# Optimization experiments

Hardware: AMD Instinct MI355X
Metric: run time of the kernel (lower is better)

Reference implementation:

```python
import jax, jax.numpy as jnp
import numpy as np

C = 96          # channels (= output_dim)
NUM_HEADS = 6
DILS = (1, 2, 3)
KS_ATT = 3      # dilate-attention kernel size
KS_COR = 5      # self-correlation kernel size
PAD_COR = 2
LN_EPS = 1e-5


def _unfold(x, k, dil, pad):
    # torch.nn.Unfold(kernel=k, dilation=dil, padding=pad, stride=1)
    # x: [B, C, H, W] -> [B, C, k*k, H, W] (channel-major, kernel row-major)
    B, c, H, W = x.shape
    xp = jnp.pad(x, ((0, 0), (0, 0), (pad, pad), (pad, pad)))
    patches = [xp[:, :, i * dil:i * dil + H, j * dil:j * dil + W]
               for i in range(k) for j in range(k)]
    return jnp.stack(patches, axis=2)


def _layernorm(x, g, b):
    m = jnp.mean(x, axis=-1, keepdims=True)
    v = jnp.mean((x - m) ** 2, axis=-1, keepdims=True)
    return (x - m) * jax.lax.rsqrt(v + LN_EPS) * g + b


def _dilate_attn(q, k, v, dil, head_dim, scale):
    # q,k,v: [B, cb, H, W] with cb = C // num_dilation
    B, cb, H, W = q.shape
    heads = cb // head_dim
    qf = q.reshape(B, heads, head_dim, H * W)                                  # bhdn
    kp = _unfold(k, KS_ATT, dil, dil).reshape(B, heads, head_dim, KS_ATT * KS_ATT, H * W)
    attn = jax.nn.softmax(jnp.einsum('bhdn,bhdkn->bhnk', qf, kp) * scale, axis=-1)
    vp = _unfold(v, KS_ATT, dil, dil).reshape(B, heads, head_dim, KS_ATT * KS_ATT, H * W)
    out = jnp.einsum('bhnk,bhdkn->bnhd', attn, vp)                             # [B,HW,heads,hd]
    return out.reshape(B, H, W, cb)


def _forward(x, g1, b1, Wqkv, bqkv, Wproj, bproj, g2, b2, W1, bm1, W2, bm2):
    B, Cc, H, W = x.shape
    nd = len(DILS)
    head_dim = Cc // NUM_HEADS
    scale = head_dim ** (-0.5)

    xh = jnp.transpose(x, (0, 2, 3, 1))                                        # [B,H,W,C]

    # --- MultiDilatelocalAttention block ---
    y = _layernorm(xh, g1, b1)
    qkv = jnp.einsum('bhwc,oc->bhwo', y, Wqkv) + bqkv                          # 1x1 conv == linear
    qkv = jnp.transpose(qkv, (0, 3, 1, 2)).reshape(B, 3, nd, Cc // nd, H, W)
    outs = []
    for i, d in enumerate(DILS):
        outs.append(_dilate_attn(qkv[:, 0, i], qkv[:, 1, i], qkv[:, 2, i], d, head_dim, scale))
    a = jnp.concatenate(outs, axis=-1)                                         # dilation-major channels
    a = a @ Wproj.T + bproj
    xh = xh + a

    # --- MLP block ---
    z = _layernorm(xh, g2, b2)
    z = jax.nn.gelu(z @ W1.T + bm1, approximate=False) @ W2.T + bm2
    xh = xh + z

    # --- self-correlation ---
    xc = jnp.transpose(xh, (0, 3, 1, 2))                                       # [B,C,H,W]
    xc = jax.nn.relu(xc)
    nrm = jnp.sqrt(jnp.sum(xc * xc, axis=1, keepdims=True))
    xc = xc / jnp.maximum(nrm, 1e-12)                                          # F.normalize dim=1
    pat = _unfold(xc, KS_COR, 1, PAD_COR)                                      # [B,C,25,H,W]
    out = pat.reshape(B, Cc, KS_COR, KS_COR, H, W) * xc[:, :, None, None]
    return jnp.transpose(out, (0, 1, 4, 5, 2, 3))                              # [B,C,H,W,5,5]


def setup_inputs() -> dict:
    key = jax.random.key(0)
    ks = jax.random.split(key, 8)
    B, H, W = 8, 64, 64
    s = 0.02
    return {
        'x': jax.random.normal(ks[0], (B, C, H, W), jnp.float32),
        'g1': jnp.ones((C,), jnp.float32),
        'b1': jnp.zeros((C,), jnp.float32),
        'Wqkv': jax.random.normal(ks[1], (3 * C, C), jnp.float32) * s,
        'bqkv': jnp.zeros((3 * C,), jnp.float32),
        'Wproj': jax.random.normal(ks[2], (C, C), jnp.float32) * s,
        'bproj': jnp.zeros((C,), jnp.float32),
        'g2': jnp.ones((C,), jnp.float32),
        'b2': jnp.zeros((C,), jnp.float32),
        'W1': jax.random.normal(ks[3], (4 * C, C), jnp.float32) * s,
        'bm1': jnp.zeros((4 * C,), jnp.float32),
        'W2': jax.random.normal(ks[4], (C, 4 * C), jnp.float32) * s,
        'bm2': jnp.zeros((C,), jnp.float32),
    }


def reference(x, g1, b1, Wqkv, bqkv, Wproj, bproj, g2, b2, W1, bm1, W2, bm2):
    return _forward(x, g1, b1, Wqkv, bqkv, Wproj, bproj, g2, b2, W1, bm1, W2, bm2)
```

## Files before the change

kernel.cpp:

```cpp
#include <hip/hip_runtime.h>
#include <math.h>

#define NN 4096
#define BN 32768
#define CSTR 66

using short8 = __attribute__((ext_vector_type(8))) short;
using f32x4  = __attribute__((ext_vector_type(4))) float;
typedef unsigned short ushort_t;

__device__ inline unsigned f2bfu(float f) {
    unsigned u = __builtin_bit_cast(unsigned, f);
    u += 0x7FFFu + ((u >> 16) & 1u);
    return u >> 16;
}
__device__ inline ushort_t f2bf(float f) { return (ushort_t)f2bfu(f); }
__device__ inline unsigned pack2(float a, float b) { return f2bfu(a) | (f2bfu(b) << 16); }
__device__ inline float bflo(unsigned u) { return __builtin_bit_cast(float, u << 16); }
__device__ inline float bfhi(unsigned u) { return __builtin_bit_cast(float, u & 0xFFFF0000u); }

__device__ inline float gelu_f(float v) {
    float xx = v * 0.70710678118654752f;
    float a  = fabsf(xx);
    float t  = 1.0f / (1.0f + 0.3275911f * a);
    float p  = t*(0.254829592f + t*(-0.284496736f + t*(1.421413741f + t*(-1.453152027f + t*1.061405429f))));
    float erfv = 1.0f - p * __expf(-xx*xx);
    erfv = copysignf(erfv, xx);
    return 0.5f * v * (1.0f + erfv);
}

__device__ inline void stage_w(const unsigned* __restrict__ wbf, int stage,
                               ushort_t* dst, int wv, int lane) {
    const unsigned* src = wbf + (long)stage * 5120 + lane * 4;
    #pragma unroll
    for (int i = 0; i < 5; ++i) {
        int chunk = wv + 4 * i;
        __builtin_amdgcn_global_load_lds(
            (const __attribute__((address_space(1))) unsigned*)(src + chunk * 256),
            (__attribute__((address_space(3))) unsigned*)(dst + chunk * 512),
            16, 0, 0);
    }
}

__device__ inline float dotk16(const unsigned* kv, const float* q) {
    const uint4 a = *(const uint4*)kv;
    const uint4 b = *(const uint4*)(kv + 4);
    float l;
    l  = q[0]*bflo(a.x)  + q[1]*bfhi(a.x);
    l += q[2]*bflo(a.y)  + q[3]*bfhi(a.y);
    l += q[4]*bflo(a.z)  + q[5]*bfhi(a.z);
    l += q[6]*bflo(a.w)  + q[7]*bfhi(a.w);
    l += q[8]*bflo(b.x)  + q[9]*bfhi(b.x);
    l += q[10]*bflo(b.y) + q[11]*bfhi(b.y);
    l += q[12]*bflo(b.z) + q[13]*bfhi(b.z);
    l += q[14]*bflo(b.w) + q[15]*bfhi(b.w);
    return l;
}
__device__ inline void accv16(const unsigned* kv, float wgt, float* o) {
    const uint4 a = *(const uint4*)kv;
    const uint4 b = *(const uint4*)(kv + 4);
    o[0]  += wgt*bflo(a.x);  o[1]  += wgt*bfhi(a.x);
    o[2]  += wgt*bflo(a.y);  o[3]  += wgt*bfhi(a.y);
    o[4]  += wgt*bflo(a.z);  o[5]  += wgt*bfhi(a.z);
    o[6]  += wgt*bflo(a.w);  o[7]  += wgt*bfhi(a.w);
    o[8]  += wgt*bflo(b.x);  o[9]  += wgt*bfhi(b.x);
    o[10] += wgt*bflo(b.y);  o[11] += wgt*bfhi(b.y);
    o[12] += wgt*bflo(b.z);  o[13] += wgt*bfhi(b.z);
    o[14] += wgt*bflo(b.w);  o[15] += wgt*bfhi(b.w);
}

#define MFMA_GEMM6(ACC, APTR, BPTR)                                              \
    _Pragma("unroll")                                                            \
    for (int kc = 0; kc < 3; ++kc) {                                             \
        short8 a_ = *(const short8*)&(APTR)[(wv*16 + ln)*104 + kc*32 + qd*8];    \
        _Pragma("unroll")                                                        \
        for (int t = 0; t < 6; ++t) {                                            \
            short8 b_ = *(const short8*)&(BPTR)[(t*16 + ln)*104 + kc*32 + qd*8]; \
            ACC[t] = __builtin_amdgcn_mfma_f32_16x16x32_bf16(a_, b_, ACC[t], 0, 0, 0); \
        }                                                                        \
    }

__global__ __launch_bounds__(256) void k0_pack(
    const float* __restrict__ Wqkv, const float* __restrict__ Wproj,
    const float* __restrict__ W1, const float* __restrict__ W2,
    unsigned* __restrict__ wbf)
{
    int d = blockIdx.x * 256 + threadIdx.x;
    int s = d / 5120, r = d - s * 5120;
    int o = r / 52, qp = r - o * 52;
    unsigned val = 0u;
    if (o < 96 && qp < 48) {
        int q = qp * 2;
        float2 w2;
        if (s == 0)      w2 = *(const float2*)&Wqkv[(long)o * 96 + q];
        else if (s == 1) w2 = *(const float2*)&Wqkv[(long)(96 + o) * 96 + q];
        else if (s == 2) w2 = *(const float2*)&Wqkv[(long)(192 + o) * 96 + q];
        else if (s == 3) w2 = *(const float2*)&Wproj[(long)o * 96 + q];
        else if (((s - 4) & 1) == 0) { int kb = (s - 4) >> 1; w2 = *(const float2*)&W1[(long)(kb * 96 + o) * 96 + q]; }
        else                         { int kb = (s - 4) >> 1; w2 = *(const float2*)&W2[(long)o * 384 + kb * 96 + q]; }
        val = pack2(w2.x, w2.y);
    }
    wbf[d] = val;
}

__global__ __launch_bounds__(256, 2) void k1_ln_qkv(
    const float* __restrict__ x, const float* __restrict__ g1, const float* __restrict__ b1,
    const float* __restrict__ bqkv, const unsigned* __restrict__ wbf,
    unsigned* __restrict__ kvt32, unsigned* __restrict__ qimg)
{
    __shared__ __align__(16) float    Cs[96 * CSTR];
    __shared__ __align__(16) ushort_t As[64 * 104];
    __shared__ __align__(16) ushort_t Bs[2][10240];
    __shared__ float lnm[64], lnr[64];
    const int tid = threadIdx.x;
    const int bid = blockIdx.x;
    const int wg  = ((bid & 7) << 6) | (bid >> 3);
    const long bn0 = (long)wg << 6;
    const int b  = (int)(bn0 >> 12);
    const int n0 = (int)(bn0 & 4095);
    const int lane = tid & 63, wv = tid >> 6;
    const int ln = lane & 15, qd = lane >> 4;

    stage_w(wbf, 0, &Bs[0][0], wv, lane);
    stage_w(wbf, 1, &Bs[1][0], wv, lane);
    for (int i = 0; i < 6; ++i) {
        int idx = i * 256 + tid;
        int c = idx >> 4, p4 = idx & 15;
        float4 v = *(const float4*)&x[((long)(b * 96 + c) << 12) + n0 + p4 * 4];
        float* dst = &Cs[c * CSTR + p4 * 4];
        dst[0] = v.x; dst[1] = v.y; dst[2] = v.z; dst[3] = v.w;
    }
    __syncthreads();
    {
        int p = tid >> 2, part = tid & 3, c0 = part * 24;
        float s = 0.f, ss = 0.f;
        for (int c = c0; c < c0 + 24; ++c) { float v = Cs[c*CSTR + p]; s += v; ss += v*v; }
        s  += __shfl_xor(s, 1);  s  += __shfl_xor(s, 2);
        ss += __shfl_xor(ss, 1); ss += __shfl_xor(ss, 2);
        float m = s * (1.f/96.f);
        float rstd = rsqrtf(ss * (1.f/96.f) - m*m + 1e-5f);
        if (part == 0) { lnm[p] = m; lnr[p] = rstd; }
    }
    __syncthreads();
    for (int i = 0; i < 12; ++i) {
        int idx = i * 256 + tid;
        int p = idx / 48, cp = idx % 48;
        float m = lnm[p], rs = lnr[p];
        int c = 2 * cp;
        *(unsigned*)&As[p * 104 + 2*cp] =
            pack2((Cs[c*CSTR + p]     - m) * rs * g1[c]   + b1[c],
                  (Cs[(c+1)*CSTR + p] - m) * rs * g1[c+1] + b1[c+1]);
    }
    __syncthreads();
    f32x4 acc[6];
    #pragma unroll
    for (int t = 0; t < 6; ++t) acc[t] = (f32x4){0.f,0.f,0.f,0.f};
    MFMA_GEMM6(acc, As, Bs[0]);
    #pragma unroll
    for (int t = 0; t < 6; ++t)
        #pragma unroll
        for (int r = 0; r < 4; ++r)
            Cs[(t*16 + ln)*CSTR + (wv*16 + qd*4 + r)] = acc[t][r];
    __syncthreads();
    stage_w(wbf, 2, &Bs[0][0], wv, lane);
    for (int i = 0; i < 13; ++i) {
        int idx = i * 256 + tid;
        int p = idx / 52, cp = idx - p * 52;
        unsigned val = 0u;
        if (cp < 48) {
            int c = 2 * cp;
            val = pack2(Cs[c*CSTR + p] + bqkv[c], Cs[(c+1)*CSTR + p] + bqkv[c+1]);
        }
        qimg[(long)wg * 3328 + idx] = val;
    }
    #pragma unroll
    for (int t = 0; t < 6; ++t) acc[t] = (f32x4){0.f,0.f,0.f,0.f};
    MFMA_GEMM6(acc, As, Bs[1]);
    __syncthreads();
    #pragma unroll
    for (int t = 0; t < 6; ++t)
        #pragma unroll
        for (int r = 0; r < 4; ++r)
            Cs[(t*16 + ln)*CSTR + (wv*16 + qd*4 + r)] = acc[t][r];
    __syncthreads();
    for (int i = 0; i < 12; ++i) {
        int idx = i * 256 + tid;
        int p = idx / 48, cp = idx % 48;
        int c = 2 * cp;
        kvt32[(bn0 + p) * 96 + cp] =
            pack2(Cs[c*CSTR + p] + bqkv[96 + c], Cs[(c+1)*CSTR + p] + bqkv[96 + c + 1]);
    }
    #pragma unroll
    for (int t = 0; t < 6; ++t) acc[t] = (f32x4){0.f,0.f,0.f,0.f};
    MFMA_GEMM6(acc, As, Bs[0]);
    __syncthreads();
    #pragma unroll
    for (int t = 0; t < 6; ++t)
        #pragma unroll
        for (int r = 0; r < 4; ++r)
            Cs[(t*16 + ln)*CSTR + (wv*16 + qd*4 + r)] = acc[t][r];
    __syncthreads();
    for (int i = 0; i < 12; ++i) {
        int idx = i * 256 + tid;
        int p = idx / 48, cp = idx % 48;
        int c = 2 * cp;
        kvt32[(bn0 + p) * 96 + 48 + cp] =
            pack2(Cs[c*CSTR + p] + bqkv[192 + c], Cs[(c+1)*CSTR + p] + bqkv[192 + c + 1]);
    }
}

__global__ __launch_bounds__(256, 2) void k2345(
    const unsigned* __restrict__ kvt32, const unsigned* __restrict__ qimg,
    const float* __restrict__ x, const unsigned* __restrict__ wbf,
    const float* __restrict__ bproj,
    const float* __restrict__ g2, const float* __restrict__ b2,
    const float* __restrict__ bm1, const float* __restrict__ bm2,
    float* __restrict__ xcn)
{
    __shared__ __align__(16) float    Cs[96 * CSTR];
    __shared__ __align__(16) ushort_t As[64 * 104];
    __shared__ __align__(16) ushort_t Bs[2][10240];
    __shared__ float lnm[64], lnr[64];
    ushort_t* Hs = (ushort_t*)Cs;
    const int tid = threadIdx.x;
    const int bid = blockIdx.x;
    const int wg  = ((bid & 7) << 6) | (bid >> 3);
    const long bn0 = (long)wg << 6;
    const int b  = (int)(bn0 >> 12);
    const int n0 = (int)(bn0 & 4095);
    const int h0 = n0 >> 6;
    const int lane = tid & 63, wv = tid >> 6;
    const int ln = lane & 15, qd = lane >> 4;

    stage_w(wbf, 3, &Bs[0][0], wv, lane);
    stage_w(wbf, 4, &Bs[1][0], wv, lane);
    {
        const unsigned* src = qimg + (long)wg * 3328 + lane * 4;
        #pragma unroll
        for (int i = 0; i < 4; ++i) {
            int chunk = wv + 4 * i;
            if (chunk < 13)
                __builtin_amdgcn_global_load_lds(
                    (const __attribute__((address_space(1))) unsigned*)(src + chunk * 256),
                    (__attribute__((address_space(3))) unsigned*)((ushort_t*)As + chunk * 512),
                    16, 0, 0);
        }
    }
    for (int i = 0; i < 6; ++i) {
        int idx = i * 256 + tid;
        int c = idx >> 4, p4 = idx & 15;
        float4 v = *(const float4*)&x[((long)(b * 96 + c) << 12) + n0 + p4 * 4];
        float* dst = &Cs[c * CSTR + p4 * 4];
        dst[0] = v.x; dst[1] = v.y; dst[2] = v.z; dst[3] = v.w;
    }
    __syncthreads();
    const unsigned* KV = kvt32 + (long)b * 4096 * 96;
    for (int it = 0; it < 2; ++it) {
        int item = it * 256 + tid;
        if (item < 384) {
            int p = item & 63;
            int r = item >> 6;
            int head = r & 1, di = r >> 1;
            int dil = di + 1;
            int cp0 = di*16 + head*8;
            int w = p;

            float q[16];
            #pragma unroll
            for (int j = 0; j < 8; ++j) {
                unsigned u = *(const unsigned*)&As[p * 104 + 2*(cp0 + j)];
                q[2*j] = bflo(u); q[2*j+1] = bfhi(u);
            }
            float logits[9];
            #pragma unroll
            for (int ki = 0; ki < 3; ++ki)
                #pragma unroll
                for (int kj = 0; kj < 3; ++kj) {
                    int hh = h0 + (ki-1)*dil, ww = w + (kj-1)*dil;
                    float l = 0.f;
                    if ((unsigned)hh < 64u && (unsigned)ww < 64u) {
                        int nn = (hh << 6) + ww;
                        l = dotk16(KV + (long)nn * 96 + cp0, q);
                    }
                    logits[ki*3 + kj] = l * 0.25f;
                }
            float m = logits[0];
            #pragma unroll
            for (int k = 1; k < 9; ++k) m = fmaxf(m, logits[k]);
            float e[9], s = 0.f;
            #pragma unroll
            for (int k = 0; k < 9; ++k) { e[k] = __expf(logits[k] - m); s += e[k]; }
            float inv = 1.f / s;
            float o[16];
            #pragma unroll
            for (int d = 0; d < 16; ++d) o[d] = 0.f;
            #pragma unroll
            for (int ki = 0; ki < 3; ++ki)
                #pragma unroll
                for (int kj = 0; kj < 3; ++kj) {
                    int hh = h0 + (ki-1)*dil, ww = w + (kj-1)*dil;
                    if ((unsigned)hh < 64u && (unsigned)ww < 64u) {
                        int nn = (hh << 6) + ww;
                        accv16(KV + (long)nn * 96 + 48 + cp0, e[ki*3 + kj] * inv, o);
                    }
                }
            #pragma unroll
            for (int j = 0; j < 8; ++j)
                *(unsigned*)&As[p * 104 + 2*(cp0 + j)] = pack2(o[2*j], o[2*j+1]);
        }
    }
    __syncthreads();
    float resid[24];
    {
        f32x4 acc[6];
        #pragma unroll
        for (int t = 0; t < 6; ++t) acc[t] = (f32x4){0.f,0.f,0.f,0.f};
        MFMA_GEMM6(acc, As, Bs[0]);
        #pragma unroll
        for (int t = 0; t < 6; ++t) {
            int oc = t*16 + ln;
            float bias = bproj[oc];
            #pragma unroll
            for (int r = 0; r < 4; ++r) {
                int p = wv*16 + qd*4 + r;
                float v = acc[t][r] + bias + Cs[oc*CSTR + p];
                resid[t*4 + r] = v;
                Cs[oc*CSTR + p] = v;
            }
        }
    }
    __syncthreads();
    stage_w(wbf, 5, &Bs[0][0], wv, lane);
    {
        int p = tid >> 2, part = tid & 3, c0 = part * 24;
        float s = 0.f, ss = 0.f;
        for (int c = c0; c < c0 + 24; ++c) { float v = Cs[c*CSTR + p]; s += v; ss += v*v; }
        s  += __shfl_xor(s, 1);  s  += __shfl_xor(s, 2);
        ss += __shfl_xor(ss, 1); ss += __shfl_xor(ss, 2);
        float m = s * (1.f/96.f);
        float rstd = rsqrtf(ss * (1.f/96.f) - m*m + 1e-5f);
        if (part == 0) { lnm[p] = m; lnr[p] = rstd; }
    }
    __syncthreads();
    for (int i = 0; i < 12; ++i) {
        int idx = i * 256 + tid;
        int p = idx / 48, cp = idx % 48;
        float m = lnm[p], rs = lnr[p];
        int c = 2 * cp;
        *(unsigned*)&As[p * 104 + 2*cp] =
            pack2((Cs[c*CSTR + p]     - m) * rs * g2[c]   + b2[c],
                  (Cs[(c+1)*CSTR + p] - m) * rs * g2[c+1] + b2[c+1]);
    }
    __syncthreads();
    f32x4 acc2[6];
    #pragma unroll
    for (int t = 0; t < 6; ++t) acc2[t] = (f32x4){0.f,0.f,0.f,0.f};
    for (int kb = 0; kb < 4; ++kb) {
        f32x4 acch[6];
        #pragma unroll
        for (int t = 0; t < 6; ++t) acch[t] = (f32x4){0.f,0.f,0.f,0.f};
        MFMA_GEMM6(acch, As, Bs[1]);
        #pragma unroll
        for (int t = 0; t < 6; ++t) {
            float bias = bm1[kb*96 + t*16 + ln];
            #pragma unroll
            for (int r = 0; r < 4; ++r)
                Hs[(wv*16 + qd*4 + r)*104 + t*16 + ln] = f2bf(gelu_f(acch[t][r] + bias));
        }
        __syncthreads();
        if (kb < 3) stage_w(wbf, 6 + 2*kb, &Bs[1][0], wv, lane);
        MFMA_GEMM6(acc2, Hs, Bs[0]);
        __syncthreads();
        if (kb < 3) stage_w(wbf, 7 + 2*kb, &Bs[0][0], wv, lane);
    }
    #pragma unroll
    for (int t = 0; t < 6; ++t) {
        int oc = t*16 + ln;
        float bias = bm2[oc];
        #pragma unroll
        for (int r = 0; r < 4; ++r) {
            int p = wv*16 + qd*4 + r;
            float v = acc2[t][r] + bias + resid[t*4 + r];
            Cs[oc*CSTR + p] = fmaxf(v, 0.f);
        }
    }
    __syncthreads();
    {
        int p = tid >> 2, part = tid & 3, c0 = part * 24;
        float ss = 0.f;
        for (int c = c0; c < c0 + 24; ++c) { float v = Cs[c*CSTR + p]; ss += v*v; }
        ss += __shfl_xor(ss, 1); ss += __shfl_xor(ss, 2);
        if (part == 0) lnr[p] = 1.f / fmaxf(sqrtf(ss), 1e-12f);
    }
    __syncthreads();
    for (int i = 0; i < 12; ++i) {
        int idx = i * 256 + tid;
        int p = idx / 48, cp = idx % 48;
        float inv = lnr[p];
        float2 v = make_float2(Cs[(2*cp)*CSTR + p] * inv, Cs[(2*cp+1)*CSTR + p] * inv);
        *(float2*)&xcn[(bn0 + p) * 96 + 2*cp] = v;
    }
}

__global__ __launch_bounds__(256) void k6_selfcorr(
    const float* __restrict__ xcn, float* __restrict__ out)
{
    __shared__ float xt[5 * 20 * 97];
    const int tid = threadIdx.x;
    const int wc = blockIdx.x;
    const int h  = blockIdx.y;
    const int b  = blockIdx.z;
    const int w0 = wc * 16;

    for (int i = 0; i < 38; ++i) {
        int idx = i * 256 + tid;
        if (idx < 9600) {
            int r = idx / (20 * 96);
            int rem = idx - r * (20 * 96);
            int wi = rem / 96, c = rem - wi * 96;
            int hh = h + r - 2, ww = w0 + wi - 2;
            float v = 0.f;
            if ((unsigned)hh < 64u && (unsigned)ww < 64u)
                v = xcn[(((long)b << 12) + (hh << 6) + ww) * 96 + c];
            xt[(r * 20 + wi) * 97 + c] = v;
        }
    }
    __syncthreads();
    f32x4* out4 = (f32x4*)out;
    const long ob4 = (long)b * 2457600 + (long)h * 400 + wc * 100;
    for (int i = 0; i < 38; ++i) {
        int idx = i * 256 + tid;
        if (idx < 9600) {
            int c = idx / 100;
            int r4 = idx - c * 100;
            f32x4 v;
            #pragma unroll
            for (int j = 0; j < 4; ++j) {
                int r = r4 * 4 + j;
                int lw = r / 25, k = r - lw * 25;
                int ki = k / 5, kj = k - ki * 5;
                float center = xt[(42 + lw) * 97 + c];
                float neigh  = xt[(ki * 20 + lw + kj) * 97 + c];
                v[j] = center * neigh;
            }
            __builtin_nontemporal_store(v, &out4[ob4 + (long)c * 25600 + r4]);
        }
    }
}

extern "C" void kernel_launch(void* const* d_in, const int* in_sizes, int n_in,
                              void* d_out, int out_size, void* d_ws, size_t ws_size,
                              hipStream_t stream)
{
    const float* x     = (const float*)d_in[0];
    const float* g1    = (const float*)d_in[1];
    const float* b1    = (const float*)d_in[2];
    const float* Wqkv  = (const float*)d_in[3];
    const float* bqkv  = (const float*)d_in[4];
    const float* Wproj = (const float*)d_in[5];
    const float* bproj = (const float*)d_in[6];
    const float* g2    = (const float*)d_in[7];
    const float* b2    = (const float*)d_in[8];
    const float* W1    = (const float*)d_in[9];
    const float* bm1   = (const float*)d_in[10];
    const float* W2    = (const float*)d_in[11];
    const float* bm2   = (const float*)d_in[12];
    float* out = (float*)d_out;

    char* w = (char*)d_ws;
    unsigned* wbf   = (unsigned*)w;  w += 12 * 20480;
    unsigned* kvt32 = (unsigned*)w;  w += (size_t)BN * 96 * 4;
    unsigned* qimg  = (unsigned*)w;  w += (size_t)512 * 3328 * 4;
    float*    xcn   = (float*)w;

    k0_pack    <<<240, 256, 0, stream>>>(Wqkv, Wproj, W1, W2, wbf);
    k1_ln_qkv  <<<BN / 64, 256, 0, stream>>>(x, g1, b1, bqkv, wbf, kvt32, qimg);
    k2345      <<<BN / 64, 256, 0, stream>>>(kvt32, qimg, x, wbf,
                                             bproj, g2, b2, bm1, bm2, xcn);
    k6_selfcorr<<<dim3(4, 64, 8), 256, 0, stream>>>(xcn, out);
}
```

Baseline: 409.6 us.

## Read GEMM weights directly from global memory instead of staging them in LDS

Removes the LDS weight buffers and the async global-to-LDS staging, and has each MFMA read its B fragments straight from the packed bf16 weights in global memory, which should stay cache resident. Freeing the 40KB of LDS lets the launch bounds rise to three blocks per CU. In the MLP loop, the hidden activations now alternate between two LDS buffers, which drops one barrier per iteration. The trade is more global and L2 load traffic plus longer MFMA operand latency, in exchange for higher occupancy and fewer synchronisations.

```diff
diff --git a/kernel.cpp b/kernel.cpp
--- a/kernel.cpp
+++ b/kernel.cpp
@@ -27,19 +27,6 @@
     float erfv = 1.0f - p * __expf(-xx*xx);
     erfv = copysignf(erfv, xx);
     return 0.5f * v * (1.0f + erfv);
-}
-
-__device__ inline void stage_w(const unsigned* __restrict__ wbf, int stage,
-                               ushort_t* dst, int wv, int lane) {
-    const unsigned* src = wbf + (long)stage * 5120 + lane * 4;
-    #pragma unroll
-    for (int i = 0; i < 5; ++i) {
-        int chunk = wv + 4 * i;
-        __builtin_amdgcn_global_load_lds(
-            (const __attribute__((address_space(1))) unsigned*)(src + chunk * 256),
-            (__attribute__((address_space(3))) unsigned*)(dst + chunk * 512),
-            16, 0, 0);
-    }
 }
 
 __device__ inline float dotk16(const unsigned* kv, const float* q) {
@@ -69,16 +56,19 @@
     o[14] += wgt*bflo(b.w);  o[15] += wgt*bfhi(b.w);
 }
 
-#define MFMA_GEMM6(ACC, APTR, BPTR)                                              \
-    _Pragma("unroll")                                                            \
-    for (int kc = 0; kc < 3; ++kc) {                                             \
-        short8 a_ = *(const short8*)&(APTR)[(wv*16 + ln)*104 + kc*32 + qd*8];    \
-        _Pragma("unroll")                                                        \
-        for (int t = 0; t < 6; ++t) {                                            \
-            short8 b_ = *(const short8*)&(BPTR)[(t*16 + ln)*104 + kc*32 + qd*8]; \
-            ACC[t] = __builtin_amdgcn_mfma_f32_16x16x32_bf16(a_, b_, ACC[t], 0, 0, 0); \
-        }                                                                        \
-    }
+__device__ inline void gemm6_g(f32x4* acc, const ushort_t* A, const unsigned* wst,
+                               int wv, int ln, int qd) {
+    #pragma unroll
+    for (int kc = 0; kc < 3; ++kc) {
+        short8 a_ = *(const short8*)&A[(wv*16 + ln)*104 + kc*32 + qd*8];
+        #pragma unroll
+        for (int t = 0; t < 6; ++t) {
+            uint4 br = *(const uint4*)&wst[(t*16 + ln)*52 + kc*16 + qd*4];
+            short8 b_ = __builtin_bit_cast(short8, br);
+            acc[t] = __builtin_amdgcn_mfma_f32_16x16x32_bf16(a_, b_, acc[t], 0, 0, 0);
+        }
+    }
+}
 
 __global__ __launch_bounds__(256) void k0_pack(
     const float* __restrict__ Wqkv, const float* __restrict__ Wproj,
@@ -103,14 +93,13 @@
     wbf[d] = val;
 }
 
-__global__ __launch_bounds__(256, 2) void k1_ln_qkv(
+__global__ __launch_bounds__(256, 3) void k1_ln_qkv(
     const float* __restrict__ x, const float* __restrict__ g1, const float* __restrict__ b1,
     const float* __restrict__ bqkv, const unsigned* __restrict__ wbf,
     unsigned* __restrict__ kvt32, unsigned* __restrict__ qimg)
 {
     __shared__ __align__(16) float    Cs[96 * CSTR];
     __shared__ __align__(16) ushort_t As[64 * 104];
-    __shared__ __align__(16) ushort_t Bs[2][10240];
     __shared__ float lnm[64], lnr[64];
     const int tid = threadIdx.x;
     const int bid = blockIdx.x;
@@ -121,8 +110,6 @@
     const int lane = tid & 63, wv = tid >> 6;
     const int ln = lane & 15, qd = lane >> 4;
 
-    stage_w(wbf, 0, &Bs[0][0], wv, lane);
-    stage_w(wbf, 1, &Bs[1][0], wv, lane);
     for (int i = 0; i < 6; ++i) {
         int idx = i * 256 + tid;
         int c = idx >> 4, p4 = idx & 15;
@@ -155,14 +142,13 @@
     f32x4 acc[6];
     #pragma unroll
     for (int t = 0; t < 6; ++t) acc[t] = (f32x4){0.f,0.f,0.f,0.f};
-    MFMA_GEMM6(acc, As, Bs[0]);
+    gemm6_g(acc, As, wbf, wv, ln, qd);
     #pragma unroll
     for (int t = 0; t < 6; ++t)
         #pragma unroll
         for (int r = 0; r < 4; ++r)
             Cs[(t*16 + ln)*CSTR + (wv*16 + qd*4 + r)] = acc[t][r];
     __syncthreads();
-    stage_w(wbf, 2, &Bs[0][0], wv, lane);
     for (int i = 0; i < 13; ++i) {
         int idx = i * 256 + tid;
         int p = idx / 52, cp = idx - p * 52;
@@ -175,7 +161,7 @@
     }
     #pragma unroll
     for (int t = 0; t < 6; ++t) acc[t] = (f32x4){0.f,0.f,0.f,0.f};
-    MFMA_GEMM6(acc, As, Bs[1]);
+    gemm6_g(acc, As, wbf + 5120, wv, ln, qd);
     __syncthreads();
     #pragma unroll
     for (int t = 0; t < 6; ++t)
@@ -192,7 +178,7 @@
     }
     #pragma unroll
     for (int t = 0; t < 6; ++t) acc[t] = (f32x4){0.f,0.f,0.f,0.f};
-    MFMA_GEMM6(acc, As, Bs[0]);
+    gemm6_g(acc, As, wbf + 2*5120, wv, ln, qd);
     __syncthreads();
     #pragma unroll
     for (int t = 0; t < 6; ++t)
@@ -209,7 +195,7 @@
     }
 }
 
-__global__ __launch_bounds__(256, 2) void k2345(
+__global__ __launch_bounds__(256, 3) void k2345(
     const unsigned* __restrict__ kvt32, const unsigned* __restrict__ qimg,
     const float* __restrict__ x, const unsigned* __restrict__ wbf,
     const float* __restrict__ bproj,
@@ -219,9 +205,9 @@
 {
     __shared__ __align__(16) float    Cs[96 * CSTR];
     __shared__ __align__(16) ushort_t As[64 * 104];
-    __shared__ __align__(16) ushort_t Bs[2][10240];
+    __shared__ __align__(16) ushort_t Hs1[64 * 104];
     __shared__ float lnm[64], lnr[64];
-    ushort_t* Hs = (ushort_t*)Cs;
+    ushort_t* Hs0 = (ushort_t*)Cs;
     const int tid = threadIdx.x;
     const int bid = blockIdx.x;
     const int wg  = ((bid & 7) << 6) | (bid >> 3);
@@ -232,8 +218,6 @@
     const int lane = tid & 63, wv = tid >> 6;
     const int ln = lane & 15, qd = lane >> 4;
 
-    stage_w(wbf, 3, &Bs[0][0], wv, lane);
-    stage_w(wbf, 4, &Bs[1][0], wv, lane);
     {
         const unsigned* src = qimg + (long)wg * 3328 + lane * 4;
         #pragma unroll
@@ -315,7 +299,7 @@
         f32x4 acc[6];
         #pragma unroll
         for (int t = 0; t < 6; ++t) acc[t] = (f32x4){0.f,0.f,0.f,0.f};
-        MFMA_GEMM6(acc, As, Bs[0]);
+        gemm6_g(acc, As, wbf + 3*5120, wv, ln, qd);
         #pragma unroll
         for (int t = 0; t < 6; ++t) {
             int oc = t*16 + ln;
@@ -330,7 +314,6 @@
         }
     }
     __syncthreads();
-    stage_w(wbf, 5, &Bs[0][0], wv, lane);
     {
         int p = tid >> 2, part = tid & 3, c0 = part * 24;
         float s = 0.f, ss = 0.f;
@@ -355,23 +338,22 @@
     f32x4 acc2[6];
     #pragma unroll
     for (int t = 0; t < 6; ++t) acc2[t] = (f32x4){0.f,0.f,0.f,0.f};
+    #pragma unroll 1
     for (int kb = 0; kb < 4; ++kb) {
+        ushort_t* H = (kb & 1) ? Hs1 : Hs0;
         f32x4 acch[6];
         #pragma unroll
         for (int t = 0; t < 6; ++t) acch[t] = (f32x4){0.f,0.f,0.f,0.f};
-        MFMA_GEMM6(acch, As, Bs[1]);
+        gemm6_g(acch, As, wbf + (4 + 2*kb)*5120, wv, ln, qd);
         #pragma unroll
         for (int t = 0; t < 6; ++t) {
             float bias = bm1[kb*96 + t*16 + ln];
             #pragma unroll
             for (int r = 0; r < 4; ++r)
-                Hs[(wv*16 + qd*4 + r)*104 + t*16 + ln] = f2bf(gelu_f(acch[t][r] + bias));
+                H[(wv*16 + qd*4 + r)*104 + t*16 + ln] = f2bf(gelu_f(acch[t][r] + bias));
         }
         __syncthreads();
-        if (kb < 3) stage_w(wbf, 6 + 2*kb, &Bs[1][0], wv, lane);
-        MFMA_GEMM6(acc2, Hs, Bs[0]);
-        __syncthreads();
-        if (kb < 3) stage_w(wbf, 7 + 2*kb, &Bs[0][0], wv, lane);
+        gemm6_g(acc2, H, wbf + (5 + 2*kb)*5120, wv, ln, qd);
     }
     #pragma unroll
     for (int t = 0; t < 6; ++t) {
```

New measurement: 448.9 us. 9.6% more time.

## Recompute Q in attention kernel, prefetch K/V neighbors into registers, vectorize selfcorr load

Applied to the files above, without the earlier changes.

The Q projection moves out of the first kernel into the fused attention/MLP kernel, where LN1 and the Q GEMM are recomputed from x. This drops the qimg workspace write and read-back. K neighbor rows for the first 256 attention items are loaded into registers before the LN/GEMM work, and V rows after it, so global-load latency overlaps with compute. The weight double-buffer slots are reassigned to match. The self-correlation tile load now uses float4 reads. In exchange, the heavier kernel repeats the LN and Q GEMM and holds many more registers, which may reduce occupancy.

```diff
diff --git a/kernel.cpp b/kernel.cpp
--- a/kernel.cpp
+++ b/kernel.cpp
@@ -42,9 +42,7 @@
     }
 }
 
-__device__ inline float dotk16(const unsigned* kv, const float* q) {
-    const uint4 a = *(const uint4*)kv;
-    const uint4 b = *(const uint4*)(kv + 4);
+__device__ inline float dotreg(const uint4& a, const uint4& b, const float* q) {
     float l;
     l  = q[0]*bflo(a.x)  + q[1]*bfhi(a.x);
     l += q[2]*bflo(a.y)  + q[3]*bfhi(a.y);
@@ -56,9 +54,7 @@
     l += q[14]*bflo(b.w) + q[15]*bfhi(b.w);
     return l;
 }
-__device__ inline void accv16(const unsigned* kv, float wgt, float* o) {
-    const uint4 a = *(const uint4*)kv;
-    const uint4 b = *(const uint4*)(kv + 4);
+__device__ inline void accreg(const uint4& a, const uint4& b, float wgt, float* o) {
     o[0]  += wgt*bflo(a.x);  o[1]  += wgt*bfhi(a.x);
     o[2]  += wgt*bflo(a.y);  o[3]  += wgt*bfhi(a.y);
     o[4]  += wgt*bflo(a.z);  o[5]  += wgt*bfhi(a.z);
@@ -103,10 +99,10 @@
     wbf[d] = val;
 }
 
-__global__ __launch_bounds__(256, 2) void k1_ln_qkv(
+__global__ __launch_bounds__(256, 2) void k1_ln_kv(
     const float* __restrict__ x, const float* __restrict__ g1, const float* __restrict__ b1,
     const float* __restrict__ bqkv, const unsigned* __restrict__ wbf,
-    unsigned* __restrict__ kvt32, unsigned* __restrict__ qimg)
+    unsigned* __restrict__ kvt32)
 {
     __shared__ __align__(16) float    Cs[96 * CSTR];
     __shared__ __align__(16) ushort_t As[64 * 104];
@@ -121,8 +117,8 @@
     const int lane = tid & 63, wv = tid >> 6;
     const int ln = lane & 15, qd = lane >> 4;
 
-    stage_w(wbf, 0, &Bs[0][0], wv, lane);
-    stage_w(wbf, 1, &Bs[1][0], wv, lane);
+    stage_w(wbf, 1, &Bs[0][0], wv, lane);
+    stage_w(wbf, 2, &Bs[1][0], wv, lane);
     for (int i = 0; i < 6; ++i) {
         int idx = i * 256 + tid;
         int c = idx >> 4, p4 = idx & 15;
@@ -162,27 +158,9 @@
         for (int r = 0; r < 4; ++r)
             Cs[(t*16 + ln)*CSTR + (wv*16 + qd*4 + r)] = acc[t][r];
     __syncthreads();
-    stage_w(wbf, 2, &Bs[0][0], wv, lane);
-    for (int i = 0; i < 13; ++i) {
-        int idx = i * 256 + tid;
-        int p = idx / 52, cp = idx - p * 52;
-        unsigned val = 0u;
-        if (cp < 48) {
-            int c = 2 * cp;
-            val = pack2(Cs[c*CSTR + p] + bqkv[c], Cs[(c+1)*CSTR + p] + bqkv[c+1]);
-        }
-        qimg[(long)wg * 3328 + idx] = val;
-    }
-    #pragma unroll
-    for (int t = 0; t < 6; ++t) acc[t] = (f32x4){0.f,0.f,0.f,0.f};
-    MFMA_GEMM6(acc, As, Bs[1]);
-    __syncthreads();
-    #pragma unroll
-    for (int t = 0; t < 6; ++t)
-        #pragma unroll
-        for (int r = 0; r < 4; ++r)
-            Cs[(t*16 + ln)*CSTR + (wv*16 + qd*4 + r)] = acc[t][r];
-    __syncthreads();
+    f32x4 accv[6];
+    #pragma unroll
+    for (int t = 0; t < 6; ++t) accv[t] = (f32x4){0.f,0.f,0.f,0.f};
     for (int i = 0; i < 12; ++i) {
         int idx = i * 256 + tid;
         int p = idx / 48, cp = idx % 48;
@@ -190,15 +168,13 @@
         kvt32[(bn0 + p) * 96 + cp] =
             pack2(Cs[c*CSTR + p] + bqkv[96 + c], Cs[(c+1)*CSTR + p] + bqkv[96 + c + 1]);
     }
-    #pragma unroll
-    for (int t = 0; t < 6; ++t) acc[t] = (f32x4){0.f,0.f,0.f,0.f};
-    MFMA_GEMM6(acc, As, Bs[0]);
+    MFMA_GEMM6(accv, As, Bs[1]);
     __syncthreads();
     #pragma unroll
     for (int t = 0; t < 6; ++t)
         #pragma unroll
         for (int r = 0; r < 4; ++r)
-            Cs[(t*16 + ln)*CSTR + (wv*16 + qd*4 + r)] = acc[t][r];
+            Cs[(t*16 + ln)*CSTR + (wv*16 + qd*4 + r)] = accv[t][r];
     __syncthreads();
     for (int i = 0; i < 12; ++i) {
         int idx = i * 256 + tid;
@@ -210,8 +186,9 @@
 }
 
 __global__ __launch_bounds__(256, 2) void k2345(
-    const unsigned* __restrict__ kvt32, const unsigned* __restrict__ qimg,
-    const float* __restrict__ x, const unsigned* __restrict__ wbf,
+    const unsigned* __restrict__ kvt32, const float* __restrict__ x,
+    const float* __restrict__ g1, const float* __restrict__ b1,
+    const float* __restrict__ bqkv, const unsigned* __restrict__ wbf,
     const float* __restrict__ bproj,
     const float* __restrict__ g2, const float* __restrict__ b2,
     const float* __restrict__ bm1, const float* __restrict__ bm2,
@@ -232,20 +209,27 @@
     const int lane = tid & 63, wv = tid >> 6;
     const int ln = lane & 15, qd = lane >> 4;
 
-    stage_w(wbf, 3, &Bs[0][0], wv, lane);
-    stage_w(wbf, 4, &Bs[1][0], wv, lane);
-    {
-        const unsigned* src = qimg + (long)wg * 3328 + lane * 4;
-        #pragma unroll
-        for (int i = 0; i < 4; ++i) {
-            int chunk = wv + 4 * i;
-            if (chunk < 13)
-                __builtin_amdgcn_global_load_lds(
-                    (const __attribute__((address_space(1))) unsigned*)(src + chunk * 256),
-                    (__attribute__((address_space(3))) unsigned*)((ushort_t*)As + chunk * 512),
-                    16, 0, 0);
-        }
-    }
+    stage_w(wbf, 0, &Bs[0][0], wv, lane);
+    stage_w(wbf, 3, &Bs[1][0], wv, lane);
+    const unsigned* KV = kvt32 + (long)b * 4096 * 96;
+    const int p0 = tid & 63, r0 = tid >> 6;
+    const int head0 = r0 & 1, di0 = r0 >> 1, dil0 = di0 + 1;
+    const int cp00 = di0*16 + head0*8;
+    uint4 kr[9][2];
+    #pragma unroll
+    for (int ki = 0; ki < 3; ++ki)
+        #pragma unroll
+        for (int kj = 0; kj < 3; ++kj) {
+            int nidx = ki*3 + kj;
+            int hh = h0 + (ki-1)*dil0, ww = p0 + (kj-1)*dil0;
+            kr[nidx][0] = (uint4){0u,0u,0u,0u};
+            kr[nidx][1] = (uint4){0u,0u,0u,0u};
+            if ((unsigned)hh < 64u && (unsigned)ww < 64u) {
+                const unsigned* src = KV + ((long)((hh << 6) + ww)) * 96 + cp00;
+                kr[nidx][0] = *(const uint4*)src;
+                kr[nidx][1] = *(const uint4*)(src + 4);
+            }
+        }
     for (int i = 0; i < 6; ++i) {
         int idx = i * 256 + tid;
         int c = idx >> 4, p4 = idx & 15;
@@ -254,83 +238,6 @@
         dst[0] = v.x; dst[1] = v.y; dst[2] = v.z; dst[3] = v.w;
     }
     __syncthreads();
-    const unsigned* KV = kvt32 + (long)b * 4096 * 96;
-    for (int it = 0; it < 2; ++it) {
-        int item = it * 256 + tid;
-        if (item < 384) {
-            int p = item & 63;
-            int r = item >> 6;
-            int head = r & 1, di = r >> 1;
-            int dil = di + 1;
-            int cp0 = di*16 + head*8;
-            int w = p;
-
-            float q[16];
-            #pragma unroll
-            for (int j = 0; j < 8; ++j) {
-                unsigned u = *(const unsigned*)&As[p * 104 + 2*(cp0 + j)];
-                q[2*j] = bflo(u); q[2*j+1] = bfhi(u);
-            }
-            float logits[9];
-            #pragma unroll
-            for (int ki = 0; ki < 3; ++ki)
-                #pragma unroll
-                for (int kj = 0; kj < 3; ++kj) {
-                    int hh = h0 + (ki-1)*dil, ww = w + (kj-1)*dil;
-                    float l = 0.f;
-                    if ((unsigned)hh < 64u && (unsigned)ww < 64u) {
-                        int nn = (hh << 6) + ww;
-                        l = dotk16(KV + (long)nn * 96 + cp0, q);
-                    }
-                    logits[ki*3 + kj] = l * 0.25f;
-                }
-            float m = logits[0];
-            #pragma unroll
-            for (int k = 1; k < 9; ++k) m = fmaxf(m, logits[k]);
-            float e[9], s = 0.f;
-            #pragma unroll
-            for (int k = 0; k < 9; ++k) { e[k] = __expf(logits[k] - m); s += e[k]; }
-            float inv = 1.f / s;
-            float o[16];
-            #pragma unroll
-            for (int d = 0; d < 16; ++d) o[d] = 0.f;
-            #pragma unroll
-            for (int ki = 0; ki < 3; ++ki)
-                #pragma unroll
-                for (int kj = 0; kj < 3; ++kj) {
-                    int hh = h0 + (ki-1)*dil, ww = w + (kj-1)*dil;
-                    if ((unsigned)hh < 64u && (unsigned)ww < 64u) {
-                        int nn = (hh << 6) + ww;
-                        accv16(KV + (long)nn * 96 + 48 + cp0, e[ki*3 + kj] * inv, o);
-                    }
-                }
-            #pragma unroll
-            for (int j = 0; j < 8; ++j)
-                *(unsigned*)&As[p * 104 + 2*(cp0 + j)] = pack2(o[2*j], o[2*j+1]);
-        }
-    }
-    __syncthreads();
-    float resid[24];
-    {
-        f32x4 acc[6];
-        #pragma unroll
-        for (int t = 0; t < 6; ++t) acc[t] = (f32x4){0.f,0.f,0.f,0.f};
-        MFMA_GEMM6(acc, As, Bs[0]);
-        #pragma unroll
-        for (int t = 0; t < 6; ++t) {
-            int oc = t*16 + ln;
-            float bias = bproj[oc];
-            #pragma unroll
-            for (int r = 0; r < 4; ++r) {
-                int p = wv*16 + qd*4 + r;
-                float v = acc[t][r] + bias + Cs[oc*CSTR + p];
-                resid[t*4 + r] = v;
-                Cs[oc*CSTR + p] = v;
-            }
-        }
-    }
-    __syncthreads();
-    stage_w(wbf, 5, &Bs[0][0], wv, lane);
     {
         int p = tid >> 2, part = tid & 3, c0 = part * 24;
         float s = 0.f, ss = 0.f;
@@ -348,6 +255,162 @@
         float m = lnm[p], rs = lnr[p];
         int c = 2 * cp;
         *(unsigned*)&As[p * 104 + 2*cp] =
+            pack2((Cs[c*CSTR + p]     - m) * rs * g1[c]   + b1[c],
+                  (Cs[(c+1)*CSTR + p] - m) * rs * g1[c+1] + b1[c+1]);
+    }
+    __syncthreads();
+    {
+        f32x4 acc[6];
+        #pragma unroll
+        for (int t = 0; t < 6; ++t) acc[t] = (f32x4){0.f,0.f,0.f,0.f};
+        MFMA_GEMM6(acc, As, Bs[0]);
+        #pragma unroll
+        for (int t = 0; t < 6; ++t) {
+            float bias = bqkv[t*16 + ln];
+            #pragma unroll
+            for (int r = 0; r < 4; ++r)
+                As[(wv*16 + qd*4 + r)*104 + t*16 + ln] = f2bf(acc[t][r] + bias);
+        }
+    }
+    __syncthreads();
+    stage_w(wbf, 4, &Bs[0][0], wv, lane);
+    {
+        uint4 vr[9][2];
+        #pragma unroll
+        for (int ki = 0; ki < 3; ++ki)
+            #pragma unroll
+            for (int kj = 0; kj < 3; ++kj) {
+                int nidx = ki*3 + kj;
+                int hh = h0 + (ki-1)*dil0, ww = p0 + (kj-1)*dil0;
+                vr[nidx][0] = (uint4){0u,0u,0u,0u};
+                vr[nidx][1] = (uint4){0u,0u,0u,0u};
+                if ((unsigned)hh < 64u && (unsigned)ww < 64u) {
+                    const unsigned* src = KV + ((long)((hh << 6) + ww)) * 96 + 48 + cp00;
+                    vr[nidx][0] = *(const uint4*)src;
+                    vr[nidx][1] = *(const uint4*)(src + 4);
+                }
+            }
+        float q[16];
+        #pragma unroll
+        for (int j = 0; j < 8; ++j) {
+            unsigned u = *(const unsigned*)&As[p0 * 104 + 2*(cp00 + j)];
+            q[2*j] = bflo(u); q[2*j+1] = bfhi(u);
+        }
+        float logits[9];
+        #pragma unroll
+        for (int k = 0; k < 9; ++k)
+            logits[k] = dotreg(kr[k][0], kr[k][1], q) * 0.25f;
+        float m = logits[0];
+        #pragma unroll
+        for (int k = 1; k < 9; ++k) m = fmaxf(m, logits[k]);
+        float e[9], s = 0.f;
+        #pragma unroll
+        for (int k = 0; k < 9; ++k) { e[k] = __expf(logits[k] - m); s += e[k]; }
+        float inv = 1.f / s;
+        float o[16];
+        #pragma unroll
+        for (int d = 0; d < 16; ++d) o[d] = 0.f;
+        #pragma unroll
+        for (int k = 0; k < 9; ++k)
+            accreg(vr[k][0], vr[k][1], e[k] * inv, o);
+        #pragma unroll
+        for (int j = 0; j < 8; ++j)
+            *(unsigned*)&As[p0 * 104 + 2*(cp00 + j)] = pack2(o[2*j], o[2*j+1]);
+    }
+    if (tid < 128) {
+        int item = 256 + tid;
+        int p = item & 63;
+        int r = item >> 6;
+        int head = r & 1, di = r >> 1;
+        int dil = di + 1;
+        int cp0 = di*16 + head*8;
+        float q[16];
+        #pragma unroll
+        for (int j = 0; j < 8; ++j) {
+            unsigned u = *(const unsigned*)&As[p * 104 + 2*(cp0 + j)];
+            q[2*j] = bflo(u); q[2*j+1] = bfhi(u);
+        }
+        float logits[9];
+        #pragma unroll
+        for (int ki = 0; ki < 3; ++ki)
+            #pragma unroll
+            for (int kj = 0; kj < 3; ++kj) {
+                int hh = h0 + (ki-1)*dil, ww = p + (kj-1)*dil;
+                float l = 0.f;
+                if ((unsigned)hh < 64u && (unsigned)ww < 64u) {
+                    const unsigned* src = KV + ((long)((hh << 6) + ww)) * 96 + cp0;
+                    uint4 a = *(const uint4*)src, bb = *(const uint4*)(src + 4);
+                    float qq[16];
+                    #pragma unroll
+                    for (int j = 0; j < 16; ++j) qq[j] = q[j];
+                    l = dotreg(a, bb, qq);
+                }
+                logits[ki*3 + kj] = l * 0.25f;
+            }
+        float m = logits[0];
+        #pragma unroll
+        for (int k = 1; k < 9; ++k) m = fmaxf(m, logits[k]);
+        float e[9], s = 0.f;
+        #pragma unroll
+        for (int k = 0; k < 9; ++k) { e[k] = __expf(logits[k] - m); s += e[k]; }
+        float inv = 1.f / s;
+        float o[16];
+        #pragma unroll
+        for (int d = 0; d < 16; ++d) o[d] = 0.f;
+        #pragma unroll
+        for (int ki = 0; ki < 3; ++ki)
+            #pragma unroll
+            for (int kj = 0; kj < 3; ++kj) {
+                int hh = h0 + (ki-1)*dil, ww = p + (kj-1)*dil;
+                if ((unsigned)hh < 64u && (unsigned)ww < 64u) {
+                    const unsigned* src = KV + ((long)((hh << 6) + ww)) * 96 + 48 + cp0;
+                    uint4 a = *(const uint4*)src, bb = *(const uint4*)(src + 4);
+                    accreg(a, bb, e[ki*3 + kj] * inv, o);
+                }
+            }
+        #pragma unroll
+        for (int j = 0; j < 8; ++j)
+            *(unsigned*)&As[p * 104 + 2*(cp0 + j)] = pack2(o[2*j], o[2*j+1]);
+    }
+    __syncthreads();
+    float resid[24];
+    {
+        f32x4 acc[6];
+        #pragma unroll
+        for (int t = 0; t < 6; ++t) acc[t] = (f32x4){0.f,0.f,0.f,0.f};
+        MFMA_GEMM6(acc, As, Bs[1]);
+        #pragma unroll
+        for (int t = 0; t < 6; ++t) {
+            int oc = t*16 + ln;
+            float bias = bproj[oc];
+            #pragma unroll
+            for (int r = 0; r < 4; ++r) {
+                int p = wv*16 + qd*4 + r;
+                float v = acc[t][r] + bias + Cs[oc*CSTR + p];
+                resid[t*4 + r] = v;
+                Cs[oc*CSTR + p] = v;
+            }
+        }
+    }
+    __syncthreads();
+    stage_w(wbf, 5, &Bs[1][0], wv, lane);
+    {
+        int p = tid >> 2, part = tid & 3, c0 = part * 24;
+        float s = 0.f, ss = 0.f;
+        for (int c = c0; c < c0 + 24; ++c) { float v = Cs[c*CSTR + p]; s += v; ss += v*v; }
+        s  += __shfl_xor(s, 1);  s  += __shfl_xor(s, 2);
+        ss += __shfl_xor(ss, 1); ss += __shfl_xor(ss, 2);
+        float m = s * (1.f/96.f);
+        float rstd = rsqrtf(ss * (1.f/96.f) - m*m + 1e-5f);
+        if (part == 0) { lnm[p] = m; lnr[p] = rstd; }
+    }
+    __syncthreads();
+    for (int i = 0; i < 12; ++i) {
+        int idx = i * 256 + tid;
+        int p = idx / 48, cp = idx % 48;
+        float m = lnm[p], rs = lnr[p];
+        int c = 2 * cp;
+        *(unsigned*)&As[p * 104 + 2*cp] =
             pack2((Cs[c*CSTR + p]     - m) * rs * g2[c]   + b2[c],
                   (Cs[(c+1)*CSTR + p] - m) * rs * g2[c+1] + b2[c+1]);
     }
@@ -359,7 +422,7 @@
         f32x4 acch[6];
         #pragma unroll
         for (int t = 0; t < 6; ++t) acch[t] = (f32x4){0.f,0.f,0.f,0.f};
-        MFMA_GEMM6(acch, As, Bs[1]);
+        MFMA_GEMM6(acch, As, Bs[0]);
         #pragma unroll
         for (int t = 0; t < 6; ++t) {
             float bias = bm1[kb*96 + t*16 + ln];
@@ -368,10 +431,10 @@
                 Hs[(wv*16 + qd*4 + r)*104 + t*16 + ln] = f2bf(gelu_f(acch[t][r] + bias));
         }
         __syncthreads();
-        if (kb < 3) stage_w(wbf, 6 + 2*kb, &Bs[1][0], wv, lane);
-        MFMA_GEMM6(acc2, Hs, Bs[0]);
+        if (kb < 3) stage_w(wbf, 6 + 2*kb, &Bs[0][0], wv, lane);
+        MFMA_GEMM6(acc2, Hs, Bs[1]);
         __syncthreads();
-        if (kb < 3) stage_w(wbf, 7 + 2*kb, &Bs[0][0], wv, lane);
+        if (kb < 3) stage_w(wbf, 7 + 2*kb, &Bs[1][0], wv, lane);
     }
     #pragma unroll
     for (int t = 0; t < 6; ++t) {
@@ -412,17 +475,19 @@
     const int b  = blockIdx.z;
     const int w0 = wc * 16;
 
-    for (int i = 0; i < 38; ++i) {
-        int idx = i * 256 + tid;
-        if (idx < 9600) {
-            int r = idx / (20 * 96);
-            int rem = idx - r * (20 * 96);
-            int wi = rem / 96, c = rem - wi * 96;
+    const f32x4* xcn4 = (const f32x4*)xcn;
+    for (int i = 0; i < 10; ++i) {
+        int idx = i * 256 + tid;
+        if (idx < 2400) {
+            int r = idx / 480;
+            int rem = idx - r * 480;
+            int wi = rem / 24, c4 = rem - wi * 24;
             int hh = h + r - 2, ww = w0 + wi - 2;
-            float v = 0.f;
+            f32x4 v = (f32x4){0.f, 0.f, 0.f, 0.f};
             if ((unsigned)hh < 64u && (unsigned)ww < 64u)
-                v = xcn[(((long)b << 12) + (hh << 6) + ww) * 96 + c];
-            xt[(r * 20 + wi) * 97 + c] = v;
+                v = xcn4[(((long)b << 12) + (hh << 6) + ww) * 24 + c4];
+            float* dst = &xt[(r * 20 + wi) * 97 + c4 * 4];
+            dst[0] = v[0]; dst[1] = v[1]; dst[2] = v[2]; dst[3] = v[3];
         }
     }
     __syncthreads();
@@ -470,12 +535,11 @@
     char* w = (char*)d_ws;
     unsigned* wbf   = (unsigned*)w;  w += 12 * 20480;
     unsigned* kvt32 = (unsigned*)w;  w += (size_t)BN * 96 * 4;
-    unsigned* qimg  = (unsigned*)w;  w += (size_t)512 * 3328 * 4;
     float*    xcn   = (float*)w;
 
     k0_pack    <<<240, 256, 0, stream>>>(Wqkv, Wproj, W1, W2, wbf);
-    k1_ln_qkv  <<<BN / 64, 256, 0, stream>>>(x, g1, b1, bqkv, wbf, kvt32, qimg);
-    k2345      <<<BN / 64, 256, 0, stream>>>(kvt32, qimg, x, wbf,
+    k1_ln_kv   <<<BN / 64, 256, 0, stream>>>(x, g1, b1, bqkv, wbf, kvt32);
+    k2345      <<<BN / 64, 256, 0, stream>>>(kvt32, x, g1, b1, bqkv, wbf,
                                              bproj, g2, b2, bm1, bm2, xcn);
     k6_selfcorr<<<dim3(4, 64, 8), 256, 0, stream>>>(xcn, out);
 }
```

Measured after the change: 415.2 us. Within noise of the previous version (+1.4%).
